# Performance work log

Measured on AMD Instinct MI355X. Metric: run time of the kernel, lower is better.

Reference implementation:

```python
import jax, jax.numpy as jnp
import numpy as np

N_NODES = 100000


def gcn_conv(x, src, dst, W, b, n_nodes):
    # PyG GCNConv: add self-loops, sym-normalize, transform then aggregate.
    loop = jnp.arange(n_nodes, dtype=src.dtype)
    s = jnp.concatenate([src, loop])
    d = jnp.concatenate([dst, loop])
    ones = jnp.ones(s.shape[0], dtype=x.dtype)
    deg = jax.ops.segment_sum(ones, d, num_segments=n_nodes)
    dinv = jnp.where(deg > 0, jax.lax.rsqrt(deg), 0.0)
    norm = dinv[s] * dinv[d]  # [E+N]
    h = x @ W                 # [N, out]
    msg = h[s] * norm[:, None]
    out = jax.ops.segment_sum(msg, d, num_segments=n_nodes)
    return out + b


def setup_inputs() -> dict:
    key = jax.random.key(0)
    ks = jax.random.split(key, 10)
    n, f = N_NODES, 128
    x = jax.random.normal(ks[0], (n, f), dtype=jnp.float32)
    edge_index = jax.random.randint(ks[1], (2, 1600000), 0, n, dtype=jnp.int64)

    def glorot(k, fin, fout):
        lim = float(np.sqrt(6.0 / (fin + fout)))
        return jax.random.uniform(k, (fin, fout), jnp.float32, -lim, lim)

    return {
        "x": x,
        "edge_index": edge_index,
        "W1": glorot(ks[2], f, 128), "b1": jnp.zeros((128,), jnp.float32),
        "W2": glorot(ks[3], 128, 64), "b2": jnp.zeros((64,), jnp.float32),
        "W3": glorot(ks[4], 64, 32), "b3": jnp.zeros((32,), jnp.float32),
        "Wc": glorot(ks[5], 64, 1), "bc": jnp.zeros((1,), jnp.float32),
    }


def reference(x, edge_index, W1, b1, W2, b2, W3, b3, Wc, bc):
    n = x.shape[0]
    src, dst = edge_index[0], edge_index[1]
    h = jax.nn.relu(gcn_conv(x, src, dst, W1, b1, n))   # dropout: eval mode
    h = jax.nn.relu(gcn_conv(h, src, dst, W2, b2, n))
    h = jax.nn.relu(gcn_conv(h, src, dst, W3, b3, n))
    edge_feat = jnp.concatenate([h[src], h[dst]], axis=1)  # [E, 64]
    return edge_feat @ Wc + bc
```

## Files before the change

### kernel.cpp

```cpp
#include <hip/hip_runtime.h>


typedef unsigned short u16;
typedef short bfrag __attribute__((ext_vector_type(8)));
typedef float ffrag __attribute__((ext_vector_type(4)));

#define BSHIFT 8
#define MAXB   512
#define BIN_CHUNK 4096
#define BCAP   4608

static __device__ __forceinline__ float4 f4add(float4 a, float4 b) {
    return make_float4(a.x + b.x, a.y + b.y, a.z + b.z, a.w + b.w);
}

static __device__ __forceinline__ u16 f2bf(float f) {
    unsigned u = __float_as_uint(f);
    u = (u + 0x7FFFu + ((u >> 16) & 1u)) >> 16;
    return (u16)u;
}

static __device__ __forceinline__ float bflo(unsigned u) {
    return __uint_as_float(u << 16);
}
static __device__ __forceinline__ float bfhi(unsigned u) {
    return __uint_as_float(u & 0xFFFF0000u);
}
static __device__ __forceinline__ void bfacc2(float& a0, float& a1, unsigned u) {
    a0 += bflo(u);
    a1 += bfhi(u);
}
static __device__ __forceinline__ void bfacc8(float* a, uint4 u) {
    bfacc2(a[0], a[1], u.x); bfacc2(a[2], a[3], u.y);
    bfacc2(a[4], a[5], u.z); bfacc2(a[6], a[7], u.w);
}


__global__ __launch_bounds__(256) void bin_edges(const int* __restrict__ src,
                                                 const int* __restrict__ dst,
                                                 int* __restrict__ bcur,
                                                 unsigned* __restrict__ pairs,
                                                 int E, int B) {
    __shared__ int h[MAXB];
    __shared__ int base[MAXB];
    const int t = threadIdx.x;
    const int e0 = blockIdx.x * BIN_CHUNK;
    const int eEnd = min(e0 + BIN_CHUNK, E);
    for (int i = t; i < B; i += 256) h[i] = 0;
    __syncthreads();
    for (int e = e0 + t; e < eEnd; e += 256)
        atomicAdd(&h[dst[e] >> BSHIFT], 1);
    __syncthreads();
    for (int i = t; i < B; i += 256) {
        int c = h[i];
        base[i] = c ? atomicAdd(&bcur[i], c) : 0;
        h[i] = 0;
    }
    __syncthreads();
    for (int e = e0 + t; e < eEnd; e += 256) {
        int d = dst[e];
        int b = d >> BSHIFT;
        int pos = base[b] + atomicAdd(&h[b], 1);
        pairs[pos] = ((unsigned)(d & 255) << 24) | (unsigned)src[e];
    }
}

__global__ __launch_bounds__(256) void build_csr(const unsigned* __restrict__ pairs,
                                                 const int* __restrict__ bcur,
                                                 int* __restrict__ rowp,
                                                 int* __restrict__ rowe,
                                                 float* __restrict__ dinv,
                                                 int* __restrict__ ssrc, int N) {
    __shared__ int s[256];
    __shared__ int cur[256];
    const int t = threadIdx.x;
    const int b = blockIdx.x;
    const int eBeg = b * BCAP, eEnd = bcur[b];
    const int nodeBase = b << BSHIFT;
    s[t] = 0;
    __syncthreads();
    for (int e = eBeg + t; e < eEnd; e += 256)
        atomicAdd(&s[pairs[e] >> 24], 1);
    __syncthreads();
    const int v = s[t];
    #pragma unroll
    for (int off = 1; off < 256; off <<= 1) {
        int add = (t >= off) ? s[t - off] : 0;
        __syncthreads();
        s[t] += add;
        __syncthreads();
    }
    const int rp = eBeg + s[t] - v;
    const int node = nodeBase + t;
    if (node < N) {
        rowp[node] = rp;
        rowe[node] = rp + v;
        dinv[node] = rsqrtf((float)(v + 1));
    }
    cur[t] = rp;
    __syncthreads();
    for (int e = eBeg + t; e < eEnd; e += 256) {
        unsigned p = pairs[e];
        int pos = atomicAdd(&cur[p >> 24], 1);
        ssrc[pos] = (int)(p & 0xFFFFFFu);
    }
}

__global__ __launch_bounds__(256) void prep_all(const float* __restrict__ W1,
                                                u16* __restrict__ w1t,
                                                const float* __restrict__ W2,
                                                u16* __restrict__ w2t,
                                                int* __restrict__ bcur, int B) {
    int idx = blockIdx.x * 256 + threadIdx.x;
    if (idx < 128 * 128) {
        int n = idx >> 7, k = idx & 127;
        w1t[idx] = f2bf(W1[k * 128 + n]);
    } else if (idx < 128 * 128 + 64 * 128) {
        int j = idx - 128 * 128;
        int n = j >> 7, k = j & 127;
        w2t[j] = f2bf(W2[k * 64 + n]);
    }
    if (idx < B) bcur[idx] = idx * BCAP;
}

template <int FIN, int FOUT, int AMODE, bool OS, int MINW>
__global__ __launch_bounds__(256, MINW)
void gemm_mfma(const void* __restrict__ Xv, const u16* __restrict__ Wt,
               const float* __restrict__ dinv, u16* __restrict__ G, int N) {
    constexpr int NT = FOUT / 16;
    constexpr int KK = FIN / 32;
    constexpr int CB = FIN / 8;
    constexpr int ITER = (64 * CB) / 256;
    __shared__ __align__(16) u16 xs[64 * FIN];
    __shared__ float ldv[64];

    const int t = threadIdx.x;
    const int wave = t >> 6;
    const int lane = t & 63;
    const int l15 = lane & 15;
    const int quad = lane >> 4;
    const int r0 = blockIdx.x * 64;

    bfrag Bf[NT][KK];
    #pragma unroll
    for (int nt = 0; nt < NT; nt++)
        #pragma unroll
        for (int kk = 0; kk < KK; kk++)
            Bf[nt][kk] = *reinterpret_cast<const bfrag*>(
                &Wt[(size_t)(nt * 16 + l15) * FIN + kk * 32 + quad * 8]);

    if (t < 64) ldv[t] = (r0 + t < N) ? dinv[r0 + t] : 0.f;

    #pragma unroll
    for (int i = 0; i < ITER; i++) {
        int v = t + 256 * i;
        int row = v / CB;
        int cb = v - row * CB;
        uint4 pack = make_uint4(0, 0, 0, 0);
        if (r0 + row < N) {
            if (AMODE == 0) {
                const float* X = (const float*)Xv;
                const float4* p = reinterpret_cast<const float4*>(
                    &X[(size_t)(r0 + row) * FIN + cb * 8]);
                float4 lo = p[0], hi = p[1];
                pack.x = f2bf(lo.x) | ((unsigned)f2bf(lo.y) << 16);
                pack.y = f2bf(lo.z) | ((unsigned)f2bf(lo.w) << 16);
                pack.z = f2bf(hi.x) | ((unsigned)f2bf(hi.y) << 16);
                pack.w = f2bf(hi.z) | ((unsigned)f2bf(hi.w) << 16);
            } else {
                const u16* X = (const u16*)Xv;
                pack = *reinterpret_cast<const uint4*>(
                    &X[((size_t)(cb >> 1) * N + (r0 + row)) * 16 + (cb & 1) * 8]);
            }
        }
        int cbs = cb ^ (row & 7);
        *reinterpret_cast<uint4*>(&xs[row * FIN + cbs * 8]) = pack;
    }
    __syncthreads();

    ffrag acc[NT];
    #pragma unroll
    for (int nt = 0; nt < NT; nt++) {
        acc[nt][0] = 0.f; acc[nt][1] = 0.f; acc[nt][2] = 0.f; acc[nt][3] = 0.f;
    }

    const int arow = wave * 16 + l15;
    #pragma unroll
    for (int kk = 0; kk < KK; kk++) {
        int cb = (kk * 4 + quad) ^ (l15 & 7);
        bfrag a = *reinterpret_cast<const bfrag*>(&xs[arow * FIN + cb * 8]);
        #pragma unroll
        for (int nt = 0; nt < NT; nt++)
            acc[nt] = __builtin_amdgcn_mfma_f32_16x16x32_bf16(a, Bf[nt][kk], acc[nt], 0, 0, 0);
    }

    #pragma unroll
    for (int nt = 0; nt < NT; nt++)
        #pragma unroll
        for (int r = 0; r < 4; r++) {
            int rl = wave * 16 + quad * 4 + r;
            int grow = r0 + rl;
            if (grow < N) {
                u16 val = f2bf(acc[nt][r] * ldv[rl]);
                if (OS)
                    G[((size_t)nt * N + grow) * 16 + l15] = val;
                else
                    G[(size_t)grow * FOUT + nt * 16 + l15] = val;
            }
        }
}

__global__ __launch_bounds__(256) void agg1_slice(const u16* __restrict__ Gs,
                                                  const int* __restrict__ rowp,
                                                  const int* __restrict__ rowe,
                                                  const int* __restrict__ ssrc,
                                                  const float* __restrict__ dinv,
                                                  const float* __restrict__ bias,
                                                  u16* __restrict__ h1s, int N) {
    const int t = threadIdx.x;
    const unsigned slice = blockIdx.x & 7;
    const int fh = t & 1;
    const int d = (blockIdx.x >> 3) * 128 + (t >> 1);
    if (d >= N) return;
    const uint4* G4 = reinterpret_cast<const uint4*>(Gs) + (size_t)slice * N * 2;

    float a[8];
    #pragma unroll
    for (int i = 0; i < 8; i++) a[i] = 0.f;
    bfacc8(a, G4[(size_t)d * 2 + fh]);

    int e = rowp[d];
    const int end = rowe[d];
    for (; e + 4 <= end; e += 4) {
        int s0 = ssrc[e], s1 = ssrc[e + 1], s2 = ssrc[e + 2], s3 = ssrc[e + 3];
        uint4 u0 = G4[(size_t)s0 * 2 + fh];
        uint4 u1 = G4[(size_t)s1 * 2 + fh];
        uint4 u2 = G4[(size_t)s2 * 2 + fh];
        uint4 u3 = G4[(size_t)s3 * 2 + fh];
        bfacc8(a, u0); bfacc8(a, u1); bfacc8(a, u2); bfacc8(a, u3);
    }
    for (; e < end; e++)
        bfacc8(a, G4[(size_t)ssrc[e] * 2 + fh]);

    const float dv = dinv[d];
    const float4 b0 = reinterpret_cast<const float4*>(bias)[slice * 4 + fh * 2];
    const float4 b1 = reinterpret_cast<const float4*>(bias)[slice * 4 + fh * 2 + 1];
    float h[8];
    h[0] = fmaxf(a[0] * dv + b0.x, 0.f);
    h[1] = fmaxf(a[1] * dv + b0.y, 0.f);
    h[2] = fmaxf(a[2] * dv + b0.z, 0.f);
    h[3] = fmaxf(a[3] * dv + b0.w, 0.f);
    h[4] = fmaxf(a[4] * dv + b1.x, 0.f);
    h[5] = fmaxf(a[5] * dv + b1.y, 0.f);
    h[6] = fmaxf(a[6] * dv + b1.z, 0.f);
    h[7] = fmaxf(a[7] * dv + b1.w, 0.f);
    uint4 pk;
    pk.x = f2bf(h[0]) | ((unsigned)f2bf(h[1]) << 16);
    pk.y = f2bf(h[2]) | ((unsigned)f2bf(h[3]) << 16);
    pk.z = f2bf(h[4]) | ((unsigned)f2bf(h[5]) << 16);
    pk.w = f2bf(h[6]) | ((unsigned)f2bf(h[7]) << 16);
    reinterpret_cast<uint4*>(h1s)[((size_t)slice * N + d) * 2 + fh] = pk;
}

__global__ __launch_bounds__(256) void agg2_gemm3(const u16* __restrict__ G,
                                                  const int* __restrict__ rowp,
                                                  const int* __restrict__ rowe,
                                                  const int* __restrict__ ssrc,
                                                  const float* __restrict__ dinv,
                                                  const float* __restrict__ bias,
                                                  const float* __restrict__ W3,
                                                  float* __restrict__ g3, int N) {
    __shared__ __align__(16) float wl[64 * 32];
    __shared__ __align__(16) float hl[32][68];
    const int t = threadIdx.x;
    {
        const float4* s4 = reinterpret_cast<const float4*>(W3);
        float4* d4 = reinterpret_cast<float4*>(wl);
        d4[t] = s4[t];
        d4[t + 256] = s4[t + 256];
    }
    __syncthreads();
    const int lj = t & 7;
    const int dn = t >> 3;
    const int d = blockIdx.x * 32 + dn;
    if (d >= N) return;

    const uint4* G4 = reinterpret_cast<const uint4*>(G);
    float a[8];
    #pragma unroll
    for (int i = 0; i < 8; i++) a[i] = 0.f;
    bfacc8(a, G4[(size_t)d * 8 + lj]);
    int e = rowp[d];
    const int end = rowe[d];
    for (; e + 8 <= end; e += 8) {
        int s0 = ssrc[e],     s1 = ssrc[e + 1], s2 = ssrc[e + 2], s3 = ssrc[e + 3];
        int s4 = ssrc[e + 4], s5 = ssrc[e + 5], s6 = ssrc[e + 6], s7 = ssrc[e + 7];
        uint4 u0 = G4[(size_t)s0 * 8 + lj];
        uint4 u1 = G4[(size_t)s1 * 8 + lj];
        uint4 u2 = G4[(size_t)s2 * 8 + lj];
        uint4 u3 = G4[(size_t)s3 * 8 + lj];
        uint4 u4 = G4[(size_t)s4 * 8 + lj];
        uint4 u5 = G4[(size_t)s5 * 8 + lj];
        uint4 u6 = G4[(size_t)s6 * 8 + lj];
        uint4 u7 = G4[(size_t)s7 * 8 + lj];
        bfacc8(a, u0); bfacc8(a, u1); bfacc8(a, u2); bfacc8(a, u3);
        bfacc8(a, u4); bfacc8(a, u5); bfacc8(a, u6); bfacc8(a, u7);
    }
    for (; e + 4 <= end; e += 4) {
        int s0 = ssrc[e], s1 = ssrc[e + 1], s2 = ssrc[e + 2], s3 = ssrc[e + 3];
        uint4 u0 = G4[(size_t)s0 * 8 + lj];
        uint4 u1 = G4[(size_t)s1 * 8 + lj];
        uint4 u2 = G4[(size_t)s2 * 8 + lj];
        uint4 u3 = G4[(size_t)s3 * 8 + lj];
        bfacc8(a, u0); bfacc8(a, u1); bfacc8(a, u2); bfacc8(a, u3);
    }
    for (; e < end; e++)
        bfacc8(a, G4[(size_t)ssrc[e] * 8 + lj]);
    const float dv = dinv[d];
    const float4 b0 = reinterpret_cast<const float4*>(bias)[lj * 2];
    const float4 b1 = reinterpret_cast<const float4*>(bias)[lj * 2 + 1];
    float h[8];
    h[0] = fmaxf(a[0] * dv + b0.x, 0.f);
    h[1] = fmaxf(a[1] * dv + b0.y, 0.f);
    h[2] = fmaxf(a[2] * dv + b0.z, 0.f);
    h[3] = fmaxf(a[3] * dv + b0.w, 0.f);
    h[4] = fmaxf(a[4] * dv + b1.x, 0.f);
    h[5] = fmaxf(a[5] * dv + b1.y, 0.f);
    h[6] = fmaxf(a[6] * dv + b1.z, 0.f);
    h[7] = fmaxf(a[7] * dv + b1.w, 0.f);
    *reinterpret_cast<float4*>(&hl[dn][lj * 8])     = make_float4(h[0], h[1], h[2], h[3]);
    *reinterpret_cast<float4*>(&hl[dn][lj * 8 + 4]) = make_float4(h[4], h[5], h[6], h[7]);
    float g[4] = {0.f, 0.f, 0.f, 0.f};
    #pragma unroll 4
    for (int k4 = 0; k4 < 16; k4++) {
        float4 hv = *reinterpret_cast<const float4*>(&hl[dn][k4 * 4]);
        float hs[4] = {hv.x, hv.y, hv.z, hv.w};
        #pragma unroll
        for (int p = 0; p < 4; p++) {
            float4 w = *reinterpret_cast<const float4*>(&wl[(k4 * 4 + p) * 32 + lj * 4]);
            g[0] += hs[p] * w.x; g[1] += hs[p] * w.y;
            g[2] += hs[p] * w.z; g[3] += hs[p] * w.w;
        }
    }
    *reinterpret_cast<float4*>(&g3[(size_t)d * 32 + lj * 4]) =
        make_float4(g[0] * dv, g[1] * dv, g[2] * dv, g[3] * dv);
}

__global__ __launch_bounds__(256) void aggregate_l3s(const float* __restrict__ G,
                                                     const int* __restrict__ rowp,
                                                     const int* __restrict__ rowe,
                                                     const int* __restrict__ ssrc,
                                                     const float* __restrict__ dinv,
                                                     const float* __restrict__ bias,
                                                     const float* __restrict__ Wc,
                                                     float2* __restrict__ ab, int N) {
    constexpr int L = 8;
    const int t = threadIdx.x;
    const int lj = t % L;
    const int d = blockIdx.x * 32 + t / L;
    if (d >= N) return;

    const float4* G4 = reinterpret_cast<const float4*>(G);
    float4 acc = G4[(size_t)d * L + lj];
    int e = rowp[d];
    const int end = rowe[d];
    for (; e + 8 <= end; e += 8) {
        int s0 = ssrc[e],     s1 = ssrc[e + 1], s2 = ssrc[e + 2], s3 = ssrc[e + 3];
        int s4 = ssrc[e + 4], s5 = ssrc[e + 5], s6 = ssrc[e + 6], s7 = ssrc[e + 7];
        float4 v0 = G4[(size_t)s0 * L + lj];
        float4 v1 = G4[(size_t)s1 * L + lj];
        float4 v2 = G4[(size_t)s2 * L + lj];
        float4 v3 = G4[(size_t)s3 * L + lj];
        float4 v4 = G4[(size_t)s4 * L + lj];
        float4 v5 = G4[(size_t)s5 * L + lj];
        float4 v6 = G4[(size_t)s6 * L + lj];
        float4 v7 = G4[(size_t)s7 * L + lj];
        acc = f4add(acc, f4add(f4add(f4add(v0, v1), f4add(v2, v3)),
                               f4add(f4add(v4, v5), f4add(v6, v7))));
    }
    for (; e + 4 <= end; e += 4) {
        int s0 = ssrc[e], s1 = ssrc[e + 1], s2 = ssrc[e + 2], s3 = ssrc[e + 3];
        float4 v0 = G4[(size_t)s0 * L + lj];
        float4 v1 = G4[(size_t)s1 * L + lj];
        float4 v2 = G4[(size_t)s2 * L + lj];
        float4 v3 = G4[(size_t)s3 * L + lj];
        acc = f4add(acc, f4add(f4add(v0, v1), f4add(v2, v3)));
    }
    for (; e < end; e++)
        acc = f4add(acc, G4[(size_t)ssrc[e] * L + lj]);
    const float dv = dinv[d];
    const float4 b4 = reinterpret_cast<const float4*>(bias)[lj];
    float4 h;
    h.x = fmaxf(acc.x * dv + b4.x, 0.f);
    h.y = fmaxf(acc.y * dv + b4.y, 0.f);
    h.z = fmaxf(acc.z * dv + b4.z, 0.f);
    h.w = fmaxf(acc.w * dv + b4.w, 0.f);
    const float4 wa = reinterpret_cast<const float4*>(Wc)[lj];
    const float4 wb = reinterpret_cast<const float4*>(Wc + 32)[lj];
    float p = h.x * wa.x + h.y * wa.y + h.z * wa.z + h.w * wa.w;
    float q = h.x * wb.x + h.y * wb.y + h.z * wb.z + h.w * wb.w;
    p += __shfl_xor(p, 1); q += __shfl_xor(q, 1);
    p += __shfl_xor(p, 2); q += __shfl_xor(q, 2);
    p += __shfl_xor(p, 4); q += __shfl_xor(q, 4);
    if (lj == 0) ab[d] = make_float2(p, q);
}


__global__ __launch_bounds__(256) void edge_out(const int* __restrict__ src,
                                                const int* __restrict__ dst,
                                                const float2* __restrict__ ab,
                                                const float* __restrict__ bc,
                                                float* __restrict__ out, int E) {
    int e = blockIdx.x * 256 + threadIdx.x;
    if (e < E) out[e] = ab[src[e]].x + ab[dst[e]].y + bc[0];
}

extern "C" void kernel_launch(void* const* d_in, const int* in_sizes, int n_in,
                              void* d_out, int out_size, void* d_ws, size_t ws_size,
                              hipStream_t stream) {
    const float* x  = (const float*)d_in[0];
    const int*   ei = (const int*)d_in[1];
    const float* W1 = (const float*)d_in[2];
    const float* b1 = (const float*)d_in[3];
    const float* W2 = (const float*)d_in[4];
    const float* b2 = (const float*)d_in[5];
    const float* W3 = (const float*)d_in[6];
    const float* b3 = (const float*)d_in[7];
    const float* Wc = (const float*)d_in[8];
    const float* bc = (const float*)d_in[9];
    float* out = (float*)d_out;

    const int N = in_sizes[0] / 128;
    const int E = in_sizes[1] / 2;
    const int B = (N + 255) >> BSHIFT;
    const int* src = ei;
    const int* dst = ei + E;

    size_t off = 0;
    auto alloc = [&](size_t bytes) -> void* {
        size_t o = (off + 255) & ~(size_t)255;
        off = o + bytes;
        return (void*)((char*)d_ws + o);
    };
    float* dinv = (float*)alloc((size_t)N * 4);
    int*   rowp = (int*)alloc((size_t)N * 4);
    int*   rowe = (int*)alloc((size_t)N * 4);
    int*   bcur = (int*)alloc((size_t)(B + 1) * 4);
    int*   ssrc = (int*)alloc((size_t)B * BCAP * 4);
    u16*   w1t  = (u16*)alloc(128 * 128 * 2);
    u16*   w2t  = (u16*)alloc(64 * 128 * 2);
    u16*   g16  = (u16*)alloc((size_t)N * 128 * 2);
    u16*   h1s  = (u16*)alloc((size_t)N * 128 * 2);
    u16*   g2b  = (u16*)alloc((size_t)N * 64 * 2);
    float2* ab  = (float2*)alloc((size_t)N * 8);
    (void)ws_size; (void)n_in; (void)out_size;

    unsigned* pairs = (unsigned*)g2b;
    float* g3f = (float*)g16;

    const int gE = (E + 255) / 256;
    const int gR = (N + 63) / 64;

    prep_all<<<96, 256, 0, stream>>>(W1, w1t, W2, w2t, bcur, B);
    bin_edges<<<(E + BIN_CHUNK - 1) / BIN_CHUNK, 256, 0, stream>>>(src, dst, bcur, pairs, E, B);
    build_csr<<<B, 256, 0, stream>>>(pairs, bcur, rowp, rowe, dinv, ssrc, N);

    gemm_mfma<128, 128, 0, true, 2><<<gR, 256, 0, stream>>>(x, w1t, dinv, g16, N);
    agg1_slice<<<8 * ((N + 127) / 128), 256, 0, stream>>>(g16, rowp, rowe, ssrc, dinv, b1, h1s, N);
    gemm_mfma<128, 64, 2, false, 2><<<gR, 256, 0, stream>>>(h1s, w2t, dinv, g2b, N);
    agg2_gemm3<<<(N + 31) / 32, 256, 0, stream>>>(g2b, rowp, rowe, ssrc, dinv, b2, W3, g3f, N);
    aggregate_l3s<<<(N + 31) / 32, 256, 0, stream>>>(g3f, rowp, rowe, ssrc, dinv, b3, Wc, ab, N);

    edge_out<<<gE, 256, 0, stream>>>(src, dst, ab, bc, out, E);
}
```

Measured before the change: 358.0 us.

## Merge weight prep into edge binning and shrink agg1 blocks to one wave

Folds the weight transpose/convert kernel into the edge binning kernel as extra blocks, and replaces the bcur initialisation with a memset plus offsets computed from bin index. This removes one kernel launch and its serialization. Separately, the layer-1 aggregation now uses 64-thread blocks covering 32 nodes instead of 256-thread blocks, aiming for finer-grained scheduling and better load balance across irregular degrees. It adds a memset call and more, smaller blocks.

```diff
diff --git a/kernel.cpp b/kernel.cpp
--- a/kernel.cpp
+++ b/kernel.cpp
@@ -35,16 +35,34 @@
     bfacc2(a[4], a[5], u.z); bfacc2(a[6], a[7], u.w);
 }
 
-
-__global__ __launch_bounds__(256) void bin_edges(const int* __restrict__ src,
-                                                 const int* __restrict__ dst,
-                                                 int* __restrict__ bcur,
-                                                 unsigned* __restrict__ pairs,
-                                                 int E, int B) {
+__global__ __launch_bounds__(256) void k_prep(const float* __restrict__ W1,
+                                              u16* __restrict__ w1t,
+                                              const float* __restrict__ W2,
+                                              u16* __restrict__ w2t,
+                                              const int* __restrict__ src,
+                                              const int* __restrict__ dst,
+                                              int* __restrict__ bcur0,
+                                              unsigned* __restrict__ pairs,
+                                              int E, int B, int BINB) {
     __shared__ int h[MAXB];
     __shared__ int base[MAXB];
     const int t = threadIdx.x;
-    const int e0 = blockIdx.x * BIN_CHUNK;
+    int bid = blockIdx.x;
+    if (bid < 96) {
+        int idx = bid * 256 + t;
+        if (idx < 128 * 128) {
+            int n = idx >> 7, k = idx & 127;
+            w1t[idx] = f2bf(W1[k * 128 + n]);
+        } else if (idx < 128 * 128 + 64 * 128) {
+            int j = idx - 128 * 128;
+            int n = j >> 7, k = j & 127;
+            w2t[j] = f2bf(W2[k * 64 + n]);
+        }
+        return;
+    }
+    bid -= 96;
+    if (bid >= BINB) return;
+    const int e0 = bid * BIN_CHUNK;
     const int eEnd = min(e0 + BIN_CHUNK, E);
     for (int i = t; i < B; i += 256) h[i] = 0;
     __syncthreads();
@@ -53,20 +71,20 @@
     __syncthreads();
     for (int i = t; i < B; i += 256) {
         int c = h[i];
-        base[i] = c ? atomicAdd(&bcur[i], c) : 0;
+        base[i] = c ? atomicAdd(&bcur0[i], c) : 0;
         h[i] = 0;
     }
     __syncthreads();
     for (int e = e0 + t; e < eEnd; e += 256) {
         int d = dst[e];
         int b = d >> BSHIFT;
-        int pos = base[b] + atomicAdd(&h[b], 1);
+        int pos = b * BCAP + base[b] + atomicAdd(&h[b], 1);
         pairs[pos] = ((unsigned)(d & 255) << 24) | (unsigned)src[e];
     }
 }
 
 __global__ __launch_bounds__(256) void build_csr(const unsigned* __restrict__ pairs,
-                                                 const int* __restrict__ bcur,
+                                                 const int* __restrict__ bcur0,
                                                  int* __restrict__ rowp,
                                                  int* __restrict__ rowe,
                                                  float* __restrict__ dinv,
@@ -75,7 +93,7 @@
     __shared__ int cur[256];
     const int t = threadIdx.x;
     const int b = blockIdx.x;
-    const int eBeg = b * BCAP, eEnd = bcur[b];
+    const int eBeg = b * BCAP, eEnd = b * BCAP + bcur0[b];
     const int nodeBase = b << BSHIFT;
     s[t] = 0;
     __syncthreads();
@@ -104,23 +122,6 @@
         int pos = atomicAdd(&cur[p >> 24], 1);
         ssrc[pos] = (int)(p & 0xFFFFFFu);
     }
-}
-
-__global__ __launch_bounds__(256) void prep_all(const float* __restrict__ W1,
-                                                u16* __restrict__ w1t,
-                                                const float* __restrict__ W2,
-                                                u16* __restrict__ w2t,
-                                                int* __restrict__ bcur, int B) {
-    int idx = blockIdx.x * 256 + threadIdx.x;
-    if (idx < 128 * 128) {
-        int n = idx >> 7, k = idx & 127;
-        w1t[idx] = f2bf(W1[k * 128 + n]);
-    } else if (idx < 128 * 128 + 64 * 128) {
-        int j = idx - 128 * 128;
-        int n = j >> 7, k = j & 127;
-        w2t[j] = f2bf(W2[k * 64 + n]);
-    }
-    if (idx < B) bcur[idx] = idx * BCAP;
 }
 
 template <int FIN, int FOUT, int AMODE, bool OS, int MINW>
@@ -210,17 +211,17 @@
         }
 }
 
-__global__ __launch_bounds__(256) void agg1_slice(const u16* __restrict__ Gs,
-                                                  const int* __restrict__ rowp,
-                                                  const int* __restrict__ rowe,
-                                                  const int* __restrict__ ssrc,
-                                                  const float* __restrict__ dinv,
-                                                  const float* __restrict__ bias,
-                                                  u16* __restrict__ h1s, int N) {
-    const int t = threadIdx.x;
+__global__ __launch_bounds__(64) void agg1_slice64(const u16* __restrict__ Gs,
+                                                   const int* __restrict__ rowp,
+                                                   const int* __restrict__ rowe,
+                                                   const int* __restrict__ ssrc,
+                                                   const float* __restrict__ dinv,
+                                                   const float* __restrict__ bias,
+                                                   u16* __restrict__ h1s, int N) {
+    const int lane = threadIdx.x;
     const unsigned slice = blockIdx.x & 7;
-    const int fh = t & 1;
-    const int d = (blockIdx.x >> 3) * 128 + (t >> 1);
+    const int fh = lane & 1;
+    const int d = (blockIdx.x >> 3) * 32 + (lane >> 1);
     if (d >= N) return;
     const uint4* G4 = reinterpret_cast<const uint4*>(Gs) + (size_t)slice * N * 2;
 
@@ -460,13 +461,17 @@
 
     const int gE = (E + 255) / 256;
     const int gR = (N + 63) / 64;
-
-    prep_all<<<96, 256, 0, stream>>>(W1, w1t, W2, w2t, bcur, B);
-    bin_edges<<<(E + BIN_CHUNK - 1) / BIN_CHUNK, 256, 0, stream>>>(src, dst, bcur, pairs, E, B);
+    const int BINB = (E + BIN_CHUNK - 1) / BIN_CHUNK;
+
+    hipMemsetAsync(bcur, 0, (size_t)(B + 1) * 4, stream);
+
+    k_prep<<<96 + BINB, 256, 0, stream>>>(W1, w1t, W2, w2t, src, dst, bcur,
+                                          pairs, E, B, BINB);
     build_csr<<<B, 256, 0, stream>>>(pairs, bcur, rowp, rowe, dinv, ssrc, N);
 
     gemm_mfma<128, 128, 0, true, 2><<<gR, 256, 0, stream>>>(x, w1t, dinv, g16, N);
-    agg1_slice<<<8 * ((N + 127) / 128), 256, 0, stream>>>(g16, rowp, rowe, ssrc, dinv, b1, h1s, N);
+    agg1_slice64<<<8 * ((N + 31) / 32), 64, 0, stream>>>(g16, rowp, rowe, ssrc,
+                                                         dinv, b1, h1s, N);
     gemm_mfma<128, 64, 2, false, 2><<<gR, 256, 0, stream>>>(h1s, w2t, dinv, g2b, N);
     agg2_gemm3<<<(N + 31) / 32, 256, 0, stream>>>(g2b, rowp, rowe, ssrc, dinv, b2, W3, g3f, N);
     aggregate_l3s<<<(N + 31) / 32, 256, 0, stream>>>(g3f, rowp, rowe, ssrc, dinv, b3, Wc, ab, N);
```

Result: no change. 356.5 us (-0.4%).
